# Optimization experiments

Hardware: AMD Instinct MI355X
Metric: run time of the kernel (lower is better)

## Reference

```python
import jax, jax.numpy as jnp
import numpy as np

B, T, J, V, D, H = 32, 400, 30, 50000, 150, 150
L = 2  # answer_token_len (boundary model: start, end)


def _gru_step(h, x, Wih, Whh, bih, bhh):
    # torch GRUCell semantics
    gi = x @ Wih.T + bih
    gh = h @ Whh.T + bhh
    ir, iz, inn = jnp.split(gi, 3, axis=-1)
    hr, hz, hn = jnp.split(gh, 3, axis=-1)
    r = jax.nn.sigmoid(ir + hr)
    z = jax.nn.sigmoid(iz + hz)
    n = jnp.tanh(inn + r * hn)
    return (1.0 - z) * n + z * h


def _gru_seq(x, Wih, Whh, bih, bhh):
    # x: [B, S, din] -> hidden sequence [B, S, h]
    h0 = jnp.zeros((x.shape[0], Whh.shape[1]), x.dtype)
    def step(h, xt):
        h = _gru_step(h, xt, Wih, Whh, bih, bhh)
        return h, h
    _, hs = jax.lax.scan(step, h0, jnp.swapaxes(x, 0, 1))
    return jnp.swapaxes(hs, 0, 1)


def _forward(context, query,
             E,
             ctx_Wih, ctx_Whh, ctx_bih, ctx_bhh,
             q_Wih, q_Whh, q_bih, q_bhh,
             Wq, Wp, Wr, w, gate_bias, attn_bias,
             m_Wih, m_Whh, m_bih, m_bhh,
             mr_Wih, mr_Whh, mr_bih, mr_bhh,
             ptr_W1, ptr_W2, ptr_v,
             d_Wih, d_Whh, d_bih, d_bhh):
    # encode context and query with GRUs
    Hp = _gru_seq(E[context], ctx_Wih, ctx_Whh, ctx_bih, ctx_bhh)  # [B,T,H]
    Hq = _gru_seq(E[query], q_Wih, q_Whh, q_bih, q_bhh)            # [B,J,H]

    whq = jnp.einsum('bjh,hk->bjk', Hq, Wq)  # precomputed query projection [B,J,H]

    def match_scan(xs, cWih, cWhh, cbih, cbhh):
        # xs: [B,T,H] context encodings (possibly time-reversed)
        def step(h, xt):
            # G_i = tanh(Wq Hq + (Wp p_i + Wr h_{i-1}) + bias)  -> [B,J,H]
            g = jnp.tanh(whq + (xt @ Wp + h @ Wr + gate_bias)[:, None, :])
            a = jax.nn.softmax(g @ w + attn_bias, axis=-1)       # [B,J]
            q = jnp.einsum('bj,bjh->bh', a, Hq)                  # attended query
            z = jnp.concatenate([xt, q], axis=-1)                # [B,2H]
            h = _gru_step(h, z, cWih, cWhh, cbih, cbhh)
            return h, h
        h0 = jnp.zeros((xs.shape[0], xs.shape[2]), xs.dtype)
        _, hs = jax.lax.scan(step, h0, jnp.swapaxes(xs, 0, 1))
        return jnp.swapaxes(hs, 0, 1)  # [B,T,H]

    Hf = match_scan(Hp, m_Wih, m_Whh, m_bih, m_bhh)              # forward direction
    Hb = match_scan(Hp[:, ::-1], mr_Wih, mr_Whh, mr_bih, mr_bhh) # reverse direction (scan order, as original)
    Hr = jnp.concatenate([Hf, Hb], axis=-1)                      # [B,T,2H]
    zero0 = jnp.zeros((Hr.shape[0], 1, Hr.shape[2]), Hr.dtype)   # initial zero state prepended
    Hr = jnp.concatenate([zero0, Hr], axis=1)                    # [B,T+1,2H]

    # boundary pointer network: L attention steps over H_r
    enc = Hr @ ptr_W1
    def ptr_step(h, _):
        s = jnp.tanh(enc + (h @ ptr_W2)[:, None, :]) @ ptr_v     # [B,T+1]
        a = jax.nn.softmax(s, axis=-1)
        c = jnp.einsum('bt,bth->bh', a, Hr)
        h = _gru_step(h, c, d_Wih, d_Whh, d_bih, d_bhh)
        return h, a
    h0 = jnp.zeros((Hr.shape[0], Hr.shape[2]), Hr.dtype)
    _, probs = jax.lax.scan(ptr_step, h0, None, length=L)
    return jnp.swapaxes(probs, 0, 1)  # [B, L, T+1]


def setup_inputs() -> dict:
    key = jax.random.key(0)
    keys = iter(jax.random.split(key, 40))
    p = lambda *s: jax.random.normal(next(keys), s, jnp.float32) * 0.05
    inp = {
        'context': jax.random.randint(next(keys), (B, T), 0, V, dtype=jnp.int32),
        'query': jax.random.randint(next(keys), (B, J), 0, V, dtype=jnp.int32),
        'E': p(V, D),
        'ctx_Wih': p(3 * H, D), 'ctx_Whh': p(3 * H, H), 'ctx_bih': p(3 * H), 'ctx_bhh': p(3 * H),
        'q_Wih': p(3 * H, D), 'q_Whh': p(3 * H, H), 'q_bih': p(3 * H), 'q_bhh': p(3 * H),
        'Wq': p(H, H), 'Wp': p(H, H), 'Wr': p(H, H), 'w': p(H),
        'gate_bias': p(H), 'attn_bias': p(),
        'm_Wih': p(3 * H, 2 * H), 'm_Whh': p(3 * H, H), 'm_bih': p(3 * H), 'm_bhh': p(3 * H),
        'mr_Wih': p(3 * H, 2 * H), 'mr_Whh': p(3 * H, H), 'mr_bih': p(3 * H), 'mr_bhh': p(3 * H),
        'ptr_W1': p(2 * H, 2 * H), 'ptr_W2': p(2 * H, 2 * H), 'ptr_v': p(2 * H),
        'd_Wih': p(6 * H, 2 * H), 'd_Whh': p(6 * H, 2 * H), 'd_bih': p(6 * H), 'd_bhh': p(6 * H),
    }
    return inp


def reference(context, query, E,
              ctx_Wih, ctx_Whh, ctx_bih, ctx_bhh,
              q_Wih, q_Whh, q_bih, q_bhh,
              Wq, Wp, Wr, w, gate_bias, attn_bias,
              m_Wih, m_Whh, m_bih, m_bhh,
              mr_Wih, mr_Whh, mr_bih, mr_bhh,
              ptr_W1, ptr_W2, ptr_v,
              d_Wih, d_Whh, d_bih, d_bhh):
    return _forward(context, query, E,
                    ctx_Wih, ctx_Whh, ctx_bih, ctx_bhh,
                    q_Wih, q_Whh, q_bih, q_bhh,
                    Wq, Wp, Wr, w, gate_bias, attn_bias,
                    m_Wih, m_Whh, m_bih, m_bhh,
                    mr_Wih, mr_Whh, mr_bih, mr_bhh,
                    ptr_W1, ptr_W2, ptr_v,
                    d_Wih, d_Whh, d_bih, d_bhh)
```

## Files before the change

### kernel.cpp

```cpp
#include <hip/hip_runtime.h>
#include <hip/hip_bf16.h>


namespace {

constexpr int NBATCH = 32;
constexpr int TLEN   = 400;
constexpr int JQ     = 30;
constexpr int T1     = 401;

__device__ __forceinline__ float sigm(float x){ return 1.f/(1.f+__expf(-x)); }
__device__ __forceinline__ float tanh_f(float x){
  float e = __expf(-2.f*fabsf(x));
  float t = (1.f-e)/(1.f+e);
  return x < 0.f ? -t : t;
}
__device__ __forceinline__ float bf2f(unsigned short u){
  union { unsigned int i; float f; } c; c.i = ((unsigned int)u)<<16; return c.f;
}

#define NW 29
struct WDesc { const void* src[NW]; int off[NW+1]; };

__global__ void sniff_kernel(const unsigned int* __restrict__ bits, int* __restrict__ flag){
  __shared__ int cnt;
  if (threadIdx.x==0) cnt = 0;
  __syncthreads();
  int hit = 0;
  #pragma unroll
  for (int i=0;i<4;i++){
    unsigned int w = bits[threadIdx.x*4+i];
    unsigned int b = (w>>8)&0x7Fu;
    if (b==0u || (b>=0x38u && b<=0x3Fu)) hit++;
  }
  atomicAdd(&cnt, hit);
  __syncthreads();
  if (threadIdx.x==0) *flag = (cnt > 768) ? 1 : 0;
}

__global__ void convert_weights_kernel(WDesc d, float* __restrict__ out, const int* __restrict__ flag){
  const int isbf = *flag;
  const int total = d.off[NW];
  for (int e = blockIdx.x*blockDim.x+threadIdx.x; e < total; e += gridDim.x*blockDim.x){
    int j = 0;
    while (e >= d.off[j+1]) j++;
    int i = e - d.off[j];
    out[e] = isbf ? bf2f(((const unsigned short*)d.src[j])[i])
                  : ((const float*)d.src[j])[i];
  }
}

__global__ void padrows_kernel(const float* __restrict__ src, float* __restrict__ dst,
                               int rows, int cols, int ldd){
  int i = blockIdx.x*blockDim.x+threadIdx.x;
  if (i >= rows*ldd) return;
  int r = i/ldd, c = i-r*ldd;
  dst[i] = (c<cols) ? src[(size_t)r*cols+c] : 0.f;
}

__global__ void build_wcat_kernel(const float* __restrict__ Whh, const float* __restrict__ Wr,
                                  float* __restrict__ Wcat){
  int i = blockIdx.x*blockDim.x+threadIdx.x;
  if (i >= 600*152) return;
  int r = i/152, c = i-r*152;
  float v = 0.f;
  if (c < 150){
    if (r < 450) v = Whh[(size_t)r*150+c];
    else         v = Wr[(size_t)c*150 + (r-450)];
  }
  Wcat[i] = v;
}

__global__ void build_msplit_kernel(const float* __restrict__ Wcat,
                                    float* __restrict__ s2q, float* __restrict__ ext){
  int i = blockIdx.x*blockDim.x+threadIdx.x;
  if (i < 24576){
    int q = i/2048, rem = i-q*2048, r = rem/4, p = rem-r*4;
    s2q[i] = Wcat[(size_t)r*152 + 104 + 4*q + p];
  } else if (i < 24576+13376){
    int k = i-24576;
    int q = k/352, rem = k-q*352, ii = rem/4, p = rem-ii*4;
    ext[k] = Wcat[(size_t)(512+ii)*152 + 4*q + p];
  }
}

__global__ void build_gsplit_kernel(const float* __restrict__ Wpad, float* __restrict__ s2q){
  int i = blockIdx.x*blockDim.x+threadIdx.x;
  if (i >= 12*452*4) return;
  int q = i/1808, rem = i-q*1808, r = rem/4, p = rem-r*4;
  s2q[i] = (r<450) ? Wpad[(size_t)r*152 + 104 + 4*q + p] : 0.f;
}

__global__ __launch_bounds__(512) void rowproj_kernel(
    const float* __restrict__ Xrows,
    const int* __restrict__ gather, const void* __restrict__ Etab, const int* __restrict__ bfflag,
    const float* __restrict__ W, const float* __restrict__ bias,
    float* __restrict__ out, int rows, int K, int inner, int mode, int ldw, int offw, int ldo)
{
  __shared__ float xs[8][304];
  const int r0 = blockIdx.x*8;
  int nr = rows - r0; if (nr > 8) nr = 8;
  if (nr <= 0) return;
  const int isbf = gather ? *bfflag : 0;
  for (int e = threadIdx.x; e < nr*inner; e += blockDim.x){
    int r = e/inner, i = e - r*inner;
    float v;
    if (gather){
      size_t base = (size_t)gather[r0+r]*inner + i;
      v = isbf ? bf2f(((const unsigned short*)Etab)[base]) : ((const float*)Etab)[base];
    } else {
      v = Xrows[(size_t)(r0+r)*inner + i];
    }
    xs[r][i] = v;
  }
  __syncthreads();
  for (int k = threadIdx.x; k < ldo; k += blockDim.x){
    if (k < K){
      float b0 = bias ? bias[k] : 0.f;
      float acc[8];
      #pragma unroll
      for (int r=0;r<8;r++) acc[r] = b0;
      if (mode==0){
        for (int i=0;i<inner;i++){
          float wv = W[(size_t)i*ldw + k];
          #pragma unroll
          for (int r=0;r<8;r++) acc[r] += xs[r][i]*wv;
        }
      } else {
        const float* wr = W + (size_t)k*ldw + offw;
        for (int i=0;i<inner;i++){
          float wv = wr[i];
          #pragma unroll
          for (int r=0;r<8;r++) acc[r] += xs[r][i]*wv;
        }
      }
      for (int r=0;r<nr;r++) out[(size_t)(r0+r)*ldo + k] = acc[r];
    } else {
      for (int r=0;r<nr;r++) out[(size_t)(r0+r)*ldo + k] = 0.f;
    }
  }
}

#define R26(M) M(0) M(1) M(2) M(3) M(4) M(5) M(6) M(7) M(8) M(9) M(10) M(11) \
               M(12) M(13) M(14) M(15) M(16) M(17) M(18) M(19) M(20) M(21) \
               M(22) M(23) M(24) M(25)
#define DECW(i) float4 w##i;
#define LDW(i)  w##i = wrow4[i];
#define FMAW(i) { float4 hq = h4[i]; \
  acc0 = fmaf(hq.x, w##i.x, acc0); acc1 = fmaf(hq.y, w##i.y, acc1); \
  acc0 = fmaf(hq.z, w##i.z, acc0); acc1 = fmaf(hq.w, w##i.w, acc1); }

__global__ __launch_bounds__(512) void gru_scan_kernel(
    const float* __restrict__ gi0, const float* __restrict__ Wp0,
    const float* __restrict__ s2q0, const float* __restrict__ bh0,
    float* __restrict__ H0, int S0,
    const float* __restrict__ gi1, const float* __restrict__ Wp1,
    const float* __restrict__ s2q1, const float* __restrict__ bh1,
    float* __restrict__ H1, int S1)
{
  const int blk = blockIdx.x;
  const float* gi; const float* Wpad; const float* s2qG; const float* bh; float* Hs; int S;
  if (blk < 32){ gi = gi0 + (size_t)blk*S0*450;  Wpad = Wp0; s2qG = s2q0; bh = bh0;
                 Hs = H0 + (size_t)blk*S0*150;   S = S0; }
  else         { int bb = blk-32;
                 gi = gi1 + (size_t)bb*S1*450;   Wpad = Wp1; s2qG = s2q1; bh = bh1;
                 Hs = H1 + (size_t)bb*S1*150;    S = S1; }
  __shared__ float4 s2W[12*452];
  __shared__ __align__(16) float h[152];
  __shared__ float gh[452];
  const int tid = threadIdx.x;

  R26(DECW)
  float br = 0.f;
  {
    const float4* wrow4 = (const float4*)(Wpad + (size_t)((tid<450)?tid:0)*152);
    R26(LDW)
    if (tid<450) br = bh[tid];
  }
  for (int e=tid; e<12*452; e+=512) s2W[e] = ((const float4*)s2qG)[e];
  if (tid < 152) h[tid] = 0.f;
  __syncthreads();
  const float4* h4 = (const float4*)h;

  for (int t=0;t<S;t++){
    float g0=0.f,g1=0.f,g2=0.f;
    if (tid < 150){
      const float* gg = gi + (size_t)t*450;
      g0 = gg[tid]; g1 = gg[150+tid]; g2 = gg[300+tid];
    }
    if (tid < 450){
      float acc0=br, acc1=0.f;
      R26(FMAW)
      #pragma unroll
      for (int q=0;q<12;q++){
        float4 wq = s2W[q*452+tid]; float4 hq = h4[26+q];
        acc0 = fmaf(hq.x, wq.x, acc0); acc1 = fmaf(hq.y, wq.y, acc1);
        acc0 = fmaf(hq.z, wq.z, acc0); acc1 = fmaf(hq.w, wq.w, acc1);
      }
      gh[tid] = acc0+acc1;
    }
    __syncthreads();
    if (tid < 150){
      float r = sigm(g0 + gh[tid]);
      float z = sigm(g1 + gh[150+tid]);
      float n = tanh_f(g2 + r*gh[300+tid]);
      float hn = (1.f-z)*n + z*h[tid];
      h[tid] = hn;
      Hs[(size_t)t*150 + tid] = hn;
    }
    __syncthreads();
  }
}

__global__ void zero_hr0_kernel(float* __restrict__ Hr){
  int idx = blockIdx.x*blockDim.x + threadIdx.x;
  if (idx < NBATCH*300){
    int b = idx/300, k = idx - 300*b;
    Hr[(size_t)b*T1*300 + k] = 0.f;
  }
}

__global__ __launch_bounds__(512) void match_scan_kernel(
    const float* __restrict__ pWp,
    const float* __restrict__ whq,
    const float* __restrict__ giXf,
    const float* __restrict__ giXr,
    const float* __restrict__ Pf,
    const float* __restrict__ Pr,
    const float* __restrict__ WcatF, const float* __restrict__ WcatR,
    const float* __restrict__ s2qF,  const float* __restrict__ s2qR,
    const float* __restrict__ extF,  const float* __restrict__ extR,
    const float* __restrict__ m_bhh, const float* __restrict__ mr_bhh,
    const float* __restrict__ wvec,
    float* __restrict__ Hr)
{
  const int b   = blockIdx.x;
  const int dir = blockIdx.y;
  const float* giX  = dir ? giXr : giXf;
  const float* P    = dir ? Pr   : Pf;
  const float* Wcat = dir ? WcatR : WcatF;
  const float* s2qG = dir ? s2qR  : s2qF;
  const float* extG = dir ? extR  : extF;
  const float* bhh  = dir ? mr_bhh : m_bhh;

  __shared__ float4 s2W[6144];
  __shared__ float4 extW[3344];
  __shared__ float extPart[480];
  __shared__ __align__(16) float h[152];
  __shared__ float ghsRaw[512];
  __shared__ __align__(16) float gis[452];
  __shared__ __align__(16) float pwS[152];
  __shared__ __align__(16) float wlS[152];
  __shared__ float sc[32], attw[32];

  const int tid  = threadIdx.x;
  const int lane = tid & 63;
  const int wv   = tid >> 6;
  const int er   = (tid < 440) ? (tid % 88) : 0;
  const int kg   = (tid < 440) ? (tid / 88) : 0;

  R26(DECW)
  float br;
  {
    const float4* wrow4 = (const float4*)(Wcat + (size_t)tid*152);
    R26(LDW)
    br = (tid < 450) ? bhh[tid] : 0.f;
  }
  for (int e=tid; e<6144; e+=512) s2W[e]  = ((const float4*)s2qG)[e];
  for (int e=tid; e<3344; e+=512) extW[e] = ((const float4*)extG)[e];
  if (tid < 152){
    h[tid] = 0.f;
    wlS[tid] = (tid<150) ? wvec[tid] : 0.f;
  }
  __syncthreads();
  const float4* h4 = (const float4*)h;

  for (int t=0;t<TLEN;t++){
    const int tt = dir ? (TLEN-1-t) : t;

    float gv = 0.f;
    if (tid < 452) gv = giX[((size_t)b*TLEN + tt)*452 + tid];
    float4 pwv;
    if (tid >= 440 && tid < 478)
      pwv = ((const float4*)(pWp + ((size_t)b*TLEN + tt)*152))[tid-440];

    {
      float acc0=br, acc1=0.f;
      R26(FMAW)
      #pragma unroll
      for (int q=0;q<12;q++){
        float4 wq = s2W[q*512+tid]; float4 hq = h4[26+q];
        acc0 = fmaf(hq.x, wq.x, acc0); acc1 = fmaf(hq.y, wq.y, acc1);
        acc0 = fmaf(hq.z, wq.z, acc0); acc1 = fmaf(hq.w, wq.w, acc1);
      }
      ghsRaw[tid] = acc0+acc1;
    }
    if (tid < 440){
      float e0=0.f, e1=0.f;
      #pragma unroll
      for (int j=0;j<8;j++){
        int q = kg*8+j;
        if (q < 38){
          float4 wq = extW[q*88+er]; float4 hq = h4[q];
          e0 = fmaf(hq.x,wq.x,e0); e1 = fmaf(hq.y,wq.y,e1);
          e0 = fmaf(hq.z,wq.z,e0); e1 = fmaf(hq.w,wq.w,e1);
        }
      }
      extPart[kg*96+er] = e0+e1;
    } else if (tid < 478){
      ((float4*)pwS)[tid-440] = pwv;
    }
    __syncthreads();

    {
      float4 b4; b4.x=b4.y=b4.z=b4.w=0.f;
      const bool bl = (lane < 38);
      if (bl){
        float4 pw4 = ((const float4*)pwS)[lane];
        int k0 = 4*lane;
        float wr[4];
        #pragma unroll
        for (int c=0;c<4;c++){
          int k = k0+c;
          int e = (k >= 62) ? (k-62) : 0;
          float ext5 = extPart[e] + extPart[96+e] + extPart[192+e]
                     + extPart[288+e] + extPart[384+e];
          wr[c] = (k < 62) ? ghsRaw[450+k] : ext5;
        }
        b4.x = pw4.x + wr[0]; b4.y = pw4.y + wr[1];
        b4.z = pw4.z + wr[2]; b4.w = pw4.w + wr[3];
      }
      #pragma unroll
      for (int jj=0;jj<4;jj++){
        int j = wv + 8*jj;
        float a = 0.f;
        if (j < JQ && bl){
          float4 q4 = ((const float4*)(whq + ((size_t)b*JQ + j)*152))[lane];
          float4 w4 = ((const float4*)wlS)[lane];
          a = w4.x*tanh_f(q4.x+b4.x);
          a = fmaf(w4.y, tanh_f(q4.y+b4.y), a);
          a = fmaf(w4.z, tanh_f(q4.z+b4.z), a);
          a = fmaf(w4.w, tanh_f(q4.w+b4.w), a);
        }
        #pragma unroll
        for (int off=32; off; off>>=1) a += __shfl_down(a, off);
        if (j < JQ && lane==0) sc[j] = a;
      }
    }
    __syncthreads();

    if (tid < 64){
      float v = (tid < JQ) ? sc[tid] : -1e30f;
      float m = v;
      #pragma unroll
      for (int off=32; off; off>>=1) m = fmaxf(m, __shfl_down(m, off));
      m = __shfl(m, 0);
      float e = (tid < JQ) ? __expf(v-m) : 0.f;
      float su = e;
      #pragma unroll
      for (int off=32; off; off>>=1) su += __shfl_down(su, off);
      su = __shfl(su, 0);
      if (tid < JQ) attw[tid] = e/su;
    }
    __syncthreads();

    if (tid < 452){
      float acc = gv;
      const float* Pb = P + (size_t)b*JQ*452 + tid;
      #pragma unroll 6
      for (int j=0;j<JQ;j++)
        acc = fmaf(attw[j], Pb[(size_t)j*452], acc);
      gis[tid] = acc;
    }
    __syncthreads();

    if (tid < 150){
      float r = sigm(gis[tid] + ghsRaw[tid]);
      float z = sigm(gis[150+tid] + ghsRaw[150+tid]);
      float n = tanh_f(gis[300+tid] + r*ghsRaw[300+tid]);
      float hn = (1.f-z)*n + z*h[tid];
      h[tid] = hn;
      Hr[((size_t)b*T1 + (t+1))*300 + dir*150 + tid] = hn;
    }
    __syncthreads();
  }
}

__global__ __launch_bounds__(512,2) void ptr_scan_kernel(
    const float* __restrict__ enc, const float* __restrict__ Hr,
    const float* __restrict__ W2, const float* __restrict__ pv,
    const float* __restrict__ dWih, const float* __restrict__ dWhh,
    const float* __restrict__ dbih, const float* __restrict__ dbhh,
    void* __restrict__ outv, const int* __restrict__ flag)
{
  const int b = blockIdx.x;
  const int tid = threadIdx.x;
  const int isbf = *flag;
  __shared__ float h[300], hW2[300], sl[T1], al[T1], c[300];
  __shared__ float gis[900], ghs[900];
  __shared__ float vl[300];
  __shared__ float red[8];
  if (tid < 300){ h[tid] = 0.f; vl[tid] = pv[tid]; }
  __syncthreads();
  for (int l=0;l<2;l++){
    if (tid < 300){
      float a0=0.f,a1=0.f;
      for (int i=0;i<300;i+=2){
        a0 += h[i]  *W2[(size_t)i*300+tid];
        a1 += h[i+1]*W2[(size_t)(i+1)*300+tid];
      }
      hW2[tid] = a0+a1;
    }
    __syncthreads();
    {
      const int wv = tid>>6, lane = tid&63;
      for (int t=wv; t<T1; t+=8){
        const float* er = enc + ((size_t)b*T1 + t)*300;
        float acc = 0.f;
        for (int k=lane; k<300; k+=64) acc += vl[k]*tanh_f(er[k] + hW2[k]);
        #pragma unroll
        for (int off=32; off; off>>=1) acc += __shfl_down(acc, off);
        if (lane==0) sl[t] = acc;
      }
    }
    __syncthreads();
    {
      float v = (tid < T1) ? sl[tid] : -1e30f;
      float m = v;
      #pragma unroll
      for (int off=32; off; off>>=1) m = fmaxf(m, __shfl_down(m, off));
      if ((tid&63)==0) red[tid>>6] = m;
      __syncthreads();
      float bm = fmaxf(fmaxf(fmaxf(red[0],red[1]),fmaxf(red[2],red[3])),
                       fmaxf(fmaxf(red[4],red[5]),fmaxf(red[6],red[7])));
      float e = (tid < T1) ? __expf(v-bm) : 0.f;
      float su = e;
      #pragma unroll
      for (int off=32; off; off>>=1) su += __shfl_down(su, off);
      __syncthreads();
      if ((tid&63)==0) red[tid>>6] = su;
      __syncthreads();
      float bs = red[0]+red[1]+red[2]+red[3]+red[4]+red[5]+red[6]+red[7];
      if (tid < T1){
        float a = e/bs;
        al[tid] = a;
        size_t oi = ((size_t)b*2 + l)*T1 + tid;
        if (isbf) ((__hip_bfloat16*)outv)[oi] = __float2bfloat16(a);
        else      ((float*)outv)[oi] = a;
      }
    }
    __syncthreads();
    if (tid < 300){
      float acc = 0.f;
      for (int t=0;t<T1;t++) acc += al[t]*Hr[((size_t)b*T1 + t)*300 + tid];
      c[tid] = acc;
    }
    __syncthreads();
    for (int k=tid; k<900; k+=blockDim.x){
      const float* wi = dWih + (size_t)k*300;
      const float* wh = dWhh + (size_t)k*300;
      float a0 = dbih[k], a1 = dbhh[k];
      for (int i=0;i<300;i++){ a0 += c[i]*wi[i]; a1 += h[i]*wh[i]; }
      gis[k] = a0; ghs[k] = a1;
    }
    __syncthreads();
    if (tid < 300){
      float r = sigm(gis[tid] + ghs[tid]);
      float z = sigm(gis[300+tid] + ghs[300+tid]);
      float n = tanh_f(gis[600+tid] + r*ghs[600+tid]);
      h[tid] = (1.f-z)*n + z*h[tid];
    }
    __syncthreads();
  }
}

}

extern "C" void kernel_launch(void* const* d_in, const int* in_sizes, int n_in,
                              void* d_out, int out_size, void* d_ws, size_t ws_size,
                              hipStream_t stream)
{
  (void)in_sizes; (void)n_in; (void)out_size; (void)ws_size;
  float* ws = (float*)d_ws;
  int* flag = (int*)d_ws;

  static const int wsz[NW] = {
    67500,67500,450,450,
    67500,67500,450,450,
    22500,22500,22500,150,150,1,
    135000,67500,450,450,
    135000,67500,450,450,
    90000,90000,300,
    270000,270000,900,900
  };
  WDesc desc;
  int cum = 0;
  for (int j=0;j<NW;j++){ desc.src[j] = d_in[3+j]; desc.off[j] = cum; cum += wsz[j]; }
  desc.off[NW] = cum;

  float* WB = ws + 16;
  const float* P_ctx_Wih = WB + desc.off[0];
  const float* P_ctx_Whh = WB + desc.off[1];
  const float* P_ctx_bih = WB + desc.off[2];
  const float* P_ctx_bhh = WB + desc.off[3];
  const float* P_q_Wih   = WB + desc.off[4];
  const float* P_q_Whh   = WB + desc.off[5];
  const float* P_q_bih   = WB + desc.off[6];
  const float* P_q_bhh   = WB + desc.off[7];
  const float* P_Wq      = WB + desc.off[8];
  const float* P_Wp      = WB + desc.off[9];
  const float* P_Wr      = WB + desc.off[10];
  const float* P_w       = WB + desc.off[11];
  const float* P_gb      = WB + desc.off[12];
  const float* P_m_Wih   = WB + desc.off[14];
  const float* P_m_Whh   = WB + desc.off[15];
  const float* P_m_bih   = WB + desc.off[16];
  const float* P_m_bhh   = WB + desc.off[17];
  const float* P_mr_Wih  = WB + desc.off[18];
  const float* P_mr_Whh  = WB + desc.off[19];
  const float* P_mr_bih  = WB + desc.off[20];
  const float* P_mr_bhh  = WB + desc.off[21];
  const float* P_W1      = WB + desc.off[22];
  const float* P_W2      = WB + desc.off[23];
  const float* P_pv      = WB + desc.off[24];
  const float* P_dWih    = WB + desc.off[25];
  const float* P_dWhh    = WB + desc.off[26];
  const float* P_dbih    = WB + desc.off[27];
  const float* P_dbhh    = WB + desc.off[28];

  size_t p = 16 + 1468512;
  float* ctxWhhP = ws + p; p += 68400;
  float* qWhhP   = ws + p; p += 68400;
  float* s2qCtx  = ws + p; p += 21696;
  float* s2qQ    = ws + p; p += 21696;
  float* WcatF   = ws + p; p += 91200;
  float* WcatR   = ws + p; p += 91200;
  float* s2qF    = ws + p; p += 24576;
  float* s2qR    = ws + p; p += 24576;
  float* extFg   = ws + p; p += 13376;
  float* extRg   = ws + p; p += 13376;

  float* ctx_gi = ws + p; p += 5760000;
  float* q_gi   = ws + p; p += 432000;
  float* HpB    = ws + p; p += 1920000;
  float* HqB    = ws + p; p += 144000;
  float* whqB   = ws + p; p += 145920;
  float* PfB    = ws + p; p += 433920;
  float* PrB    = ws + p; p += 433920;
  float* pWpB   = ws + p; p += 1945600;
  float* giXfB  = ws + p; p += 5785600;
  float* giXrB  = ws + p; p += 5785600;
  float* HrB    = ws + p; p += 3849600;
  float* encB   = ctx_gi;

  sniff_kernel<<<1,256,0,stream>>>((const unsigned int*)d_in[2], flag);
  convert_weights_kernel<<<512,256,0,stream>>>(desc, WB, flag);
  padrows_kernel<<<(450*152+255)/256,256,0,stream>>>(P_ctx_Whh, ctxWhhP, 450,150,152);
  padrows_kernel<<<(450*152+255)/256,256,0,stream>>>(P_q_Whh,   qWhhP,   450,150,152);
  build_gsplit_kernel<<<(12*452*4+255)/256,256,0,stream>>>(ctxWhhP, s2qCtx);
  build_gsplit_kernel<<<(12*452*4+255)/256,256,0,stream>>>(qWhhP,   s2qQ);
  build_wcat_kernel<<<(600*152+255)/256,256,0,stream>>>(P_m_Whh,  P_Wr, WcatF);
  build_wcat_kernel<<<(600*152+255)/256,256,0,stream>>>(P_mr_Whh, P_Wr, WcatR);
  build_msplit_kernel<<<(24576+13376+255)/256,256,0,stream>>>(WcatF, s2qF, extFg);
  build_msplit_kernel<<<(24576+13376+255)/256,256,0,stream>>>(WcatR, s2qR, extRg);

  rowproj_kernel<<<1600,512,0,stream>>>(nullptr,(const int*)d_in[0], d_in[2], flag,
                                        P_ctx_Wih, P_ctx_bih, ctx_gi, 12800,450,150,1,150,0,450);
  rowproj_kernel<<<120,512,0,stream>>>(nullptr,(const int*)d_in[1], d_in[2], flag,
                                       P_q_Wih, P_q_bih, q_gi, 960,450,150,1,150,0,450);

  gru_scan_kernel<<<64,512,0,stream>>>(ctx_gi, ctxWhhP, s2qCtx, P_ctx_bhh, HpB, 400,
                                       q_gi,   qWhhP,   s2qQ,   P_q_bhh,   HqB, 30);

  rowproj_kernel<<<120,192,0,stream>>>(HqB,nullptr,nullptr,nullptr, P_Wq, nullptr,
                                       whqB, 960,150,150,0,150,0,152);
  rowproj_kernel<<<120,512,0,stream>>>(HqB,nullptr,nullptr,nullptr, P_m_Wih, nullptr,
                                       PfB, 960,450,150,1,300,150,452);
  rowproj_kernel<<<120,512,0,stream>>>(HqB,nullptr,nullptr,nullptr, P_mr_Wih, nullptr,
                                       PrB, 960,450,150,1,300,150,452);
  rowproj_kernel<<<1600,192,0,stream>>>(HpB,nullptr,nullptr,nullptr, P_Wp, P_gb,
                                        pWpB, 12800,150,150,0,150,0,152);
  rowproj_kernel<<<1600,512,0,stream>>>(HpB,nullptr,nullptr,nullptr, P_m_Wih, P_m_bih,
                                        giXfB, 12800,450,150,1,300,0,452);
  rowproj_kernel<<<1600,512,0,stream>>>(HpB,nullptr,nullptr,nullptr, P_mr_Wih, P_mr_bih,
                                        giXrB, 12800,450,150,1,300,0,452);

  zero_hr0_kernel<<<(NBATCH*300+511)/512,512,0,stream>>>(HrB);
  match_scan_kernel<<<dim3(NBATCH,2),512,0,stream>>>(pWpB, whqB, giXfB, giXrB,
                                                     PfB, PrB, WcatF, WcatR,
                                                     s2qF, s2qR, extFg, extRg,
                                                     P_m_bhh, P_mr_bhh, P_w, HrB);

  rowproj_kernel<<<1604,320,0,stream>>>(HrB,nullptr,nullptr,nullptr, P_W1, nullptr,
                                        encB, 12832,300,300,0,300,0,300);
  ptr_scan_kernel<<<32,512,0,stream>>>(encB, HrB, P_W2, P_pv,
                                       P_dWih, P_dWhh, P_dbih, P_dbhh, d_out, flag);
}
```

Measured before the change: 3.610 ms.

## Pre-transpose projection weights and process 16 rows per block in rowproj

The projection kernel now handles 16 rows per block and reads the input rows with float4 loads from shared memory, so each weight load is reused across twice as many rows. Weights that were read row-strided (mode 1) are transposed once up front into column-major buffers, which makes every weight access coalesced. The match scan also stores its partial Wr-products into one padded shared buffer and reduces them with float4 reads instead of scalar gathers. The costs are extra transpose launches, more workspace, and higher register pressure from 16 accumulators per thread.

```diff
diff --git a/kernel.cpp b/kernel.cpp
--- a/kernel.cpp
+++ b/kernel.cpp
@@ -58,6 +58,14 @@
   dst[i] = (c<cols) ? src[(size_t)r*cols+c] : 0.f;
 }
 
+__global__ void transpose_kernel(const float* __restrict__ src, float* __restrict__ dst,
+                                 int R, int C, int lds_, int offs){
+  int idx = blockIdx.x*blockDim.x+threadIdx.x;
+  if (idx >= R*C) return;
+  int i = idx / R, k = idx - i*R;
+  dst[(size_t)i*R + k] = src[(size_t)k*lds_ + offs + i];
+}
+
 __global__ void build_wcat_kernel(const float* __restrict__ Whh, const float* __restrict__ Wr,
                                   float* __restrict__ Wcat){
   int i = blockIdx.x*blockDim.x+threadIdx.x;
@@ -91,18 +99,18 @@
   s2q[i] = (r<450) ? Wpad[(size_t)r*152 + 104 + 4*q + p] : 0.f;
 }
 
-__global__ __launch_bounds__(512) void rowproj_kernel(
+__global__ __launch_bounds__(512) void rowproj16_kernel(
     const float* __restrict__ Xrows,
     const int* __restrict__ gather, const void* __restrict__ Etab, const int* __restrict__ bfflag,
     const float* __restrict__ W, const float* __restrict__ bias,
-    float* __restrict__ out, int rows, int K, int inner, int mode, int ldw, int offw, int ldo)
+    float* __restrict__ out, int rows, int K, int inner, int ldw, int ldo)
 {
-  __shared__ float xs[8][304];
-  const int r0 = blockIdx.x*8;
-  int nr = rows - r0; if (nr > 8) nr = 8;
+  __shared__ __align__(16) float xs[16][304];
+  const int r0 = blockIdx.x*16;
+  int nr = rows - r0; if (nr > 16) nr = 16;
   if (nr <= 0) return;
   const int isbf = gather ? *bfflag : 0;
-  for (int e = threadIdx.x; e < nr*inner; e += blockDim.x){
+  for (int e = threadIdx.x; e < nr*inner; e += 512){
     int r = e/inner, i = e - r*inner;
     float v;
     if (gather){
@@ -114,31 +122,35 @@
     xs[r][i] = v;
   }
   __syncthreads();
-  for (int k = threadIdx.x; k < ldo; k += blockDim.x){
-    if (k < K){
-      float b0 = bias ? bias[k] : 0.f;
-      float acc[8];
-      #pragma unroll
-      for (int r=0;r<8;r++) acc[r] = b0;
-      if (mode==0){
-        for (int i=0;i<inner;i++){
-          float wv = W[(size_t)i*ldw + k];
-          #pragma unroll
-          for (int r=0;r<8;r++) acc[r] += xs[r][i]*wv;
-        }
-      } else {
-        const float* wr = W + (size_t)k*ldw + offw;
-        for (int i=0;i<inner;i++){
-          float wv = wr[i];
-          #pragma unroll
-          for (int r=0;r<8;r++) acc[r] += xs[r][i]*wv;
-        }
-      }
-      for (int r=0;r<nr;r++) out[(size_t)(r0+r)*ldo + k] = acc[r];
-    } else {
-      for (int r=0;r<nr;r++) out[(size_t)(r0+r)*ldo + k] = 0.f;
-    }
-  }
+  for (int k = threadIdx.x; k < K; k += 512){
+    float b0 = bias ? bias[k] : 0.f;
+    float acc[16];
+    #pragma unroll
+    for (int r=0;r<16;r++) acc[r] = b0;
+    int i = 0;
+    for (; i+4 <= inner; i += 4){
+      float w0 = W[(size_t)i*ldw + k];
+      float w1 = W[(size_t)(i+1)*ldw + k];
+      float w2 = W[(size_t)(i+2)*ldw + k];
+      float w3 = W[(size_t)(i+3)*ldw + k];
+      #pragma unroll
+      for (int r=0;r<16;r++){
+        float4 xv = *(const float4*)&xs[r][i];
+        acc[r] = fmaf(xv.x, w0, acc[r]);
+        acc[r] = fmaf(xv.y, w1, acc[r]);
+        acc[r] = fmaf(xv.z, w2, acc[r]);
+        acc[r] = fmaf(xv.w, w3, acc[r]);
+      }
+    }
+    for (; i < inner; i++){
+      float wv = W[(size_t)i*ldw + k];
+      #pragma unroll
+      for (int r=0;r<16;r++) acc[r] = fmaf(xs[r][i], wv, acc[r]);
+    }
+    for (int r=0;r<nr;r++) out[(size_t)(r0+r)*ldo + k] = acc[r];
+  }
+  for (int k = K + threadIdx.x; k < ldo; k += 512)
+    for (int r=0;r<nr;r++) out[(size_t)(r0+r)*ldo + k] = 0.f;
 }
 
 #define R26(M) M(0) M(1) M(2) M(3) M(4) M(5) M(6) M(7) M(8) M(9) M(10) M(11) \
@@ -245,7 +257,7 @@
 
   __shared__ float4 s2W[6144];
   __shared__ float4 extW[3344];
-  __shared__ float extPart[480];
+  __shared__ __align__(16) float wrP[760];
   __shared__ __align__(16) float h[152];
   __shared__ float ghsRaw[512];
   __shared__ __align__(16) float gis[452];
@@ -268,12 +280,14 @@
   }
   for (int e=tid; e<6144; e+=512) s2W[e]  = ((const float4*)s2qG)[e];
   for (int e=tid; e<3344; e+=512) extW[e] = ((const float4*)extG)[e];
+  if (tid < 760) wrP[tid] = 0.f;
   if (tid < 152){
     h[tid] = 0.f;
     wlS[tid] = (tid<150) ? wvec[tid] : 0.f;
   }
   __syncthreads();
   const float4* h4 = (const float4*)h;
+  const float4* wrP4 = (const float4*)wrP;
 
   for (int t=0;t<TLEN;t++){
     const int tt = dir ? (TLEN-1-t) : t;
@@ -293,7 +307,9 @@
         acc0 = fmaf(hq.x, wq.x, acc0); acc1 = fmaf(hq.y, wq.y, acc1);
         acc0 = fmaf(hq.z, wq.z, acc0); acc1 = fmaf(hq.w, wq.w, acc1);
       }
-      ghsRaw[tid] = acc0+acc1;
+      float v = acc0+acc1;
+      ghsRaw[tid] = v;
+      if (tid >= 450) wrP[tid-450] = v;
     }
     if (tid < 440){
       float e0=0.f, e1=0.f;
@@ -306,10 +322,9 @@
           e0 = fmaf(hq.z,wq.z,e0); e1 = fmaf(hq.w,wq.w,e1);
         }
       }
-      extPart[kg*96+er] = e0+e1;
-    } else if (tid < 478){
-      ((float4*)pwS)[tid-440] = pwv;
-    }
+      wrP[kg*152 + 62 + er] = e0+e1;
+    }
+    if (tid >= 440 && tid < 478) ((float4*)pwS)[tid-440] = pwv;
     __syncthreads();
 
     {
@@ -317,18 +332,13 @@
       const bool bl = (lane < 38);
       if (bl){
         float4 pw4 = ((const float4*)pwS)[lane];
-        int k0 = 4*lane;
-        float wr[4];
-        #pragma unroll
-        for (int c=0;c<4;c++){
-          int k = k0+c;
-          int e = (k >= 62) ? (k-62) : 0;
-          float ext5 = extPart[e] + extPart[96+e] + extPart[192+e]
-                     + extPart[288+e] + extPart[384+e];
-          wr[c] = (k < 62) ? ghsRaw[450+k] : ext5;
-        }
-        b4.x = pw4.x + wr[0]; b4.y = pw4.y + wr[1];
-        b4.z = pw4.z + wr[2]; b4.w = pw4.w + wr[3];
+        float4 s0 = wrP4[lane],        s1 = wrP4[38+lane];
+        float4 s2 = wrP4[76+lane],     s3 = wrP4[114+lane];
+        float4 s4 = wrP4[152+lane];
+        b4.x = pw4.x + s0.x+s1.x+s2.x+s3.x+s4.x;
+        b4.y = pw4.y + s0.y+s1.y+s2.y+s3.y+s4.y;
+        b4.z = pw4.z + s0.z+s1.z+s2.z+s3.z+s4.z;
+        b4.w = pw4.w + s0.w+s1.w+s2.w+s3.w+s4.w;
       }
       #pragma unroll
       for (int jj=0;jj<4;jj++){
@@ -539,6 +549,12 @@
   float* s2qR    = ws + p; p += 24576;
   float* extFg   = ws + p; p += 13376;
   float* extRg   = ws + p; p += 13376;
+  float* ctxWihT = ws + p; p += 67500;
+  float* qWihT   = ws + p; p += 67500;
+  float* mXfT    = ws + p; p += 67500;
+  float* mXrT    = ws + p; p += 67500;
+  float* mQfT    = ws + p; p += 67500;
+  float* mQrT    = ws + p; p += 67500;
 
   float* ctx_gi = ws + p; p += 5760000;
   float* q_gi   = ws + p; p += 432000;
@@ -563,27 +579,33 @@
   build_wcat_kernel<<<(600*152+255)/256,256,0,stream>>>(P_mr_Whh, P_Wr, WcatR);
   build_msplit_kernel<<<(24576+13376+255)/256,256,0,stream>>>(WcatF, s2qF, extFg);
   build_msplit_kernel<<<(24576+13376+255)/256,256,0,stream>>>(WcatR, s2qR, extRg);
-
-  rowproj_kernel<<<1600,512,0,stream>>>(nullptr,(const int*)d_in[0], d_in[2], flag,
-                                        P_ctx_Wih, P_ctx_bih, ctx_gi, 12800,450,150,1,150,0,450);
-  rowproj_kernel<<<120,512,0,stream>>>(nullptr,(const int*)d_in[1], d_in[2], flag,
-                                       P_q_Wih, P_q_bih, q_gi, 960,450,150,1,150,0,450);
+  transpose_kernel<<<(67500+255)/256,256,0,stream>>>(P_ctx_Wih, ctxWihT, 450,150,150,0);
+  transpose_kernel<<<(67500+255)/256,256,0,stream>>>(P_q_Wih,   qWihT,   450,150,150,0);
+  transpose_kernel<<<(67500+255)/256,256,0,stream>>>(P_m_Wih,   mXfT,    450,150,300,0);
+  transpose_kernel<<<(67500+255)/256,256,0,stream>>>(P_mr_Wih,  mXrT,    450,150,300,0);
+  transpose_kernel<<<(67500+255)/256,256,0,stream>>>(P_m_Wih,   mQfT,    450,150,300,150);
+  transpose_kernel<<<(67500+255)/256,256,0,stream>>>(P_mr_Wih,  mQrT,    450,150,300,150);
+
+  rowproj16_kernel<<<800,512,0,stream>>>(nullptr,(const int*)d_in[0], d_in[2], flag,
+                                         ctxWihT, P_ctx_bih, ctx_gi, 12800,450,150,450,450);
+  rowproj16_kernel<<<60,512,0,stream>>>(nullptr,(const int*)d_in[1], d_in[2], flag,
+                                        qWihT, P_q_bih, q_gi, 960,450,150,450,450);
 
   gru_scan_kernel<<<64,512,0,stream>>>(ctx_gi, ctxWhhP, s2qCtx, P_ctx_bhh, HpB, 400,
                                        q_gi,   qWhhP,   s2qQ,   P_q_bhh,   HqB, 30);
 
-  rowproj_kernel<<<120,192,0,stream>>>(HqB,nullptr,nullptr,nullptr, P_Wq, nullptr,
-                                       whqB, 960,150,150,0,150,0,152);
-  rowproj_kernel<<<120,512,0,stream>>>(HqB,nullptr,nullptr,nullptr, P_m_Wih, nullptr,
-                                       PfB, 960,450,150,1,300,150,452);
-  rowproj_kernel<<<120,512,0,stream>>>(HqB,nullptr,nullptr,nullptr, P_mr_Wih, nullptr,
-                                       PrB, 960,450,150,1,300,150,452);
-  rowproj_kernel<<<1600,192,0,stream>>>(HpB,nullptr,nullptr,nullptr, P_Wp, P_gb,
-                                        pWpB, 12800,150,150,0,150,0,152);
-  rowproj_kernel<<<1600,512,0,stream>>>(HpB,nullptr,nullptr,nullptr, P_m_Wih, P_m_bih,
-                                        giXfB, 12800,450,150,1,300,0,452);
-  rowproj_kernel<<<1600,512,0,stream>>>(HpB,nullptr,nullptr,nullptr, P_mr_Wih, P_mr_bih,
-                                        giXrB, 12800,450,150,1,300,0,452);
+  rowproj16_kernel<<<60,512,0,stream>>>(HqB,nullptr,nullptr,nullptr, P_Wq, nullptr,
+                                        whqB, 960,150,150,150,152);
+  rowproj16_kernel<<<60,512,0,stream>>>(HqB,nullptr,nullptr,nullptr, mQfT, nullptr,
+                                        PfB, 960,450,150,450,452);
+  rowproj16_kernel<<<60,512,0,stream>>>(HqB,nullptr,nullptr,nullptr, mQrT, nullptr,
+                                        PrB, 960,450,150,450,452);
+  rowproj16_kernel<<<800,512,0,stream>>>(HpB,nullptr,nullptr,nullptr, P_Wp, P_gb,
+                                         pWpB, 12800,150,150,150,152);
+  rowproj16_kernel<<<800,512,0,stream>>>(HpB,nullptr,nullptr,nullptr, mXfT, P_m_bih,
+                                         giXfB, 12800,450,150,450,452);
+  rowproj16_kernel<<<800,512,0,stream>>>(HpB,nullptr,nullptr,nullptr, mXrT, P_mr_bih,
+                                         giXrB, 12800,450,150,450,452);
 
   zero_hr0_kernel<<<(NBATCH*300+511)/512,512,0,stream>>>(HrB);
   match_scan_kernel<<<dim3(NBATCH,2),512,0,stream>>>(pWpB, whqB, giXfB, giXrB,
@@ -591,8 +613,8 @@
                                                      s2qF, s2qR, extFg, extRg,
                                                      P_m_bhh, P_mr_bhh, P_w, HrB);
 
-  rowproj_kernel<<<1604,320,0,stream>>>(HrB,nullptr,nullptr,nullptr, P_W1, nullptr,
-                                        encB, 12832,300,300,0,300,0,300);
+  rowproj16_kernel<<<802,512,0,stream>>>(HrB,nullptr,nullptr,nullptr, P_W1, nullptr,
+                                         encB, 12832,300,300,300,300);
   ptr_scan_kernel<<<32,512,0,stream>>>(encB, HrB, P_W2, P_pv,
                                        P_dWih, P_dWhh, P_dbih, P_dbhh, d_out, flag);
 }
```

After: 3.527 ms. 2.3% less time.
